# Kernel tuning notes

Measured on AMD Instinct MI355X. Metric: run time of the kernel, lower is better.

Reference implementation:

```python
import jax, jax.numpy as jnp
import numpy as np

B, N = 8, 2048          # clouds x points per cloud
M1, M2 = 1024, 256      # centroids after ratio 0.5, then 0.25
K = 64                  # max_num_neighbors
R1, R2 = 0.2, 0.4       # radii
CURV_K = 10             # knn for curvature
CURV_SCALAR = 10.0      # Net(curvature_scalar)
NEG = -1e30


def _sqdist(a, b):
    # squared pairwise distances [len(a), len(b)] without an [.,.,3] intermediate
    return jnp.sum(a * a, -1)[:, None] + jnp.sum(b * b, -1)[None, :] - 2.0 * (a @ b.T)


def _mlp3(x, Wa, ba, Wb, bb, Wc, bc):
    # torch_geometric MLP: Linear+ReLU hidden layers, plain last layer
    h = jax.nn.relu(x @ Wa + ba)
    h = jax.nn.relu(h @ Wb + bb)
    return h @ Wc + bc


def _curvature(pos):
    # per-point surface variation lambda_min / sum(lambda) over k-NN covariance
    d2 = _sqdist(pos, pos)                        # [N,N]
    _, idx = jax.lax.top_k(-d2, CURV_K)           # k nearest (incl. self)
    nbr = pos[idx]                                # [N,k,3]
    c = nbr - jnp.mean(nbr, 1, keepdims=True)
    cov = jnp.einsum('nki,nkj->nij', c, c) / CURV_K
    ev = jnp.linalg.eigvalsh(cov)                 # ascending
    return ev[:, 0] / (jnp.sum(ev, -1) + 1e-8)


def _fps_weighted(pos, curv, m):
    # farthest point sampling, min-distance score weighted by curvature
    w = 1.0 + CURV_SCALAR * curv
    d0 = jnp.sum((pos - pos[0]) ** 2, -1)
    def step(min_d2, _):
        i = jnp.argmax(min_d2 * w)
        nd = jnp.sum((pos - pos[i]) ** 2, -1)
        return jnp.minimum(min_d2, nd), i
    _, rest = jax.lax.scan(step, d0, None, length=m - 1)
    return jnp.concatenate([jnp.zeros((1,), rest.dtype), rest])


def _sa(x, pos, curv, m, r, params):
    # SAModule: weighted FPS -> radius grouping (cap K) -> PointNetConv (gather, MLP, max)
    idx = _fps_weighted(pos, curv, m)
    cpos = pos[idx]                               # [m,3]
    d2 = _sqdist(cpos, pos)                       # [m,N]
    score = jnp.where(d2 <= r * r, -d2, NEG)
    vals, nidx = jax.lax.top_k(score, K)          # up to K nearest within radius
    mask = vals > NEG * 0.5                       # [m,K]
    rel = pos[nidx] - cpos[:, None, :]            # [m,K,3]
    feats = rel if x is None else jnp.concatenate([x[nidx], rel], -1)
    msg = _mlp3(feats, *params)                   # [m,K,F]
    msg = jnp.where(mask[:, :, None], msg, NEG)
    out = jnp.max(msg, 1)                         # scatter-max aggregation
    out = jnp.where(jnp.any(mask, 1)[:, None], out, 0.0)  # empty groups -> 0
    return out, cpos, curv[idx]


def _forward(pos, W1a, b1a, W1b, b1b, W1c, b1c, W2a, b2a, W2b, b2b, W2c, b2c,
             W3a, b3a, W3b, b3b, W3c, b3c, Wh1, bh1, Wh2, bh2, Wh3, bh3):
    p1 = (W1a, b1a, W1b, b1b, W1c, b1c)
    p2 = (W2a, b2a, W2b, b2b, W2c, b2c)
    p3 = (W3a, b3a, W3b, b3b, W3c, b3c)
    def cloud(p):
        curv = _curvature(p)
        x1, pos1, c1 = _sa(None, p, curv, M1, R1, p1)
        x2, pos2, _ = _sa(x1, pos1, c1, M2, R2, p2)
        g = _mlp3(jnp.concatenate([x2, pos2], -1), *p3)   # [M2,1024]
        return jnp.max(g, 0)                              # global max pool
    gfeat = jax.vmap(cloud)(pos.reshape(B, N, 3))          # [B,1024]
    logits = _mlp3(gfeat, Wh1, bh1, Wh2, bh2, Wh3, bh3)    # dropout (eval) = id
    return jax.nn.log_softmax(logits, -1)


_LAYERS = [("W1a", "b1a", 3, 64), ("W1b", "b1b", 64, 64), ("W1c", "b1c", 64, 128),
           ("W2a", "b2a", 131, 128), ("W2b", "b2b", 128, 128), ("W2c", "b2c", 128, 256),
           ("W3a", "b3a", 259, 256), ("W3b", "b3b", 256, 512), ("W3c", "b3c", 512, 1024),
           ("Wh1", "bh1", 1024, 512), ("Wh2", "bh2", 512, 256), ("Wh3", "bh3", 256, 10)]


def setup_inputs() -> dict:
    key = jax.random.key(0)
    ks = iter(jax.random.split(key, 2 * len(_LAYERS) + 1))
    inp = {"pos": jax.random.uniform(next(ks), (B * N, 3), jnp.float32)}
    for wn, bn, fi, fo in _LAYERS:
        inp[wn] = jax.random.normal(next(ks), (fi, fo), jnp.float32) / np.sqrt(fi)
        inp[bn] = jnp.zeros((fo,), jnp.float32)
    return inp


def reference(pos, W1a, b1a, W1b, b1b, W1c, b1c, W2a, b2a, W2b, b2b, W2c, b2c,
              W3a, b3a, W3b, b3b, W3c, b3c, Wh1, bh1, Wh2, bh2, Wh3, bh3):
    return _forward(pos, W1a, b1a, W1b, b1b, W1c, b1c, W2a, b2a, W2b, b2b, W2c, b2c,
                    W3a, b3a, W3b, b3b, W3c, b3c, Wh1, bh1, Wh2, bh2, Wh3, bh3)
```

## Files before the change

kernel.cpp:

```cpp
#include <hip/hip_runtime.h>
#include <hip/hip_fp16.h>
#include <math.h>

#define TID threadIdx.x

typedef _Float16 h2vec __attribute__((ext_vector_type(2)));
typedef _Float16 f16x8 __attribute__((ext_vector_type(8)));
typedef float f32x4 __attribute__((ext_vector_type(4)));
typedef float f32x2v __attribute__((ext_vector_type(2)));

#if __has_builtin(__builtin_elementwise_fma)
#define EFMA(a, b, c) __builtin_elementwise_fma((a), (b), (c))
#else
static __device__ __forceinline__ f32x2v EFMA(f32x2v a, f32x2v b, f32x2v c) {
    f32x2v r;
    r.x = fmaf(a.x, b.x, c.x);
    r.y = fmaf(a.y, b.y, c.y);
    return r;
}
#endif

static __device__ __forceinline__ float fdot2(unsigned a, unsigned b, float c) {
    h2vec av, bv;
    __builtin_memcpy(&av, &a, 4);
    __builtin_memcpy(&bv, &b, 4);
    return __builtin_amdgcn_fdot2(av, bv, c, false);
}

static __device__ __forceinline__ unsigned packh2(float a, float b) {
    __half2 hh = __floats2half2_rn(a, b);
    unsigned u;
    __builtin_memcpy(&u, &hh, 4);
    return u;
}

static __device__ __forceinline__ unsigned encf(float f) {
    unsigned u = __float_as_uint(f);
    return (u >> 31) ? ~u : (u | 0x80000000u);
}
static __device__ __forceinline__ float decf(unsigned e) {
    unsigned u = (e >> 31) ? (e & 0x7fffffffu) : ~e;
    return __uint_as_float(u);
}

static __device__ __forceinline__ int wave_sum(int v) {
    v += __builtin_amdgcn_update_dpp(0, v, 0x111, 0xf, 0xf, true);
    v += __builtin_amdgcn_update_dpp(0, v, 0x112, 0xf, 0xf, true);
    v += __builtin_amdgcn_update_dpp(0, v, 0x114, 0xf, 0xf, true);
    v += __builtin_amdgcn_update_dpp(0, v, 0x118, 0xf, 0xf, true);
    v += __builtin_amdgcn_update_dpp(0, v, 0x142, 0xf, 0xf, true);
    v += __builtin_amdgcn_update_dpp(0, v, 0x143, 0xf, 0xf, true);
    return __builtin_amdgcn_readlane(v, 63);
}

template <int CTRL>
static __device__ __forceinline__ unsigned long long dpp_max_u64(unsigned long long k) {
    int lo = (int)(unsigned)(k & 0xffffffffULL);
    int hi = (int)(unsigned)(k >> 32);
    int lo2 = __builtin_amdgcn_update_dpp(0, lo, CTRL, 0xf, 0xf, true);
    int hi2 = __builtin_amdgcn_update_dpp(0, hi, CTRL, 0xf, 0xf, true);
    unsigned long long k2 = ((unsigned long long)(unsigned)hi2 << 32) | (unsigned)lo2;
    return k2 > k ? k2 : k;
}

static __device__ __forceinline__ void pack_slot(const float* __restrict__ W,
                                                 unsigned* __restrict__ out,
                                                 int K, int ncols, int t) {
    int lane = t & 63;
    int frag = t >> 6;
    int nct = ncols >> 4;
    int ks = frag / nct, ct = frag - ks * nct;
    int kbase = (ks << 5) + ((lane >> 4) << 3);
    int cc = (ct << 4) + (lane & 15);
    unsigned o[4];
#pragma unroll
    for (int i = 0; i < 4; ++i) {
        int k0 = kbase + 2 * i, k1 = kbase + 2 * i + 1;
        float f0 = (k0 < K) ? W[(size_t)k0 * ncols + cc] : 0.f;
        float f1 = (k1 < K) ? W[(size_t)k1 * ncols + cc] : 0.f;
        o[i] = packh2(f0, f1);
    }
    *(uint4*)&out[(size_t)t * 4] = make_uint4(o[0], o[1], o[2], o[3]);
}

__global__ __launch_bounds__(256) void curv_kernel(const float* __restrict__ pos,
                                                   float* __restrict__ curv) {
    __shared__ float4 sp[2048];
    __shared__ float smd[64][40];
    __shared__ int smi[64][40];
    int cloud = blockIdx.x >> 5;
    int base = cloud << 11;
    for (int j = TID; j < 2048; j += 256) {
        const float* p = pos + (size_t)(base + j) * 3;
        float x = p[0], y = p[1], z = p[2];
        sp[j] = make_float4(x, y, z, fmaf(x, x, fmaf(y, y, z * z)));
    }
    __syncthreads();
    int pt = TID >> 2;
    int sub = TID & 3;
    int li = ((blockIdx.x & 31) << 6) + pt;
    float4 pi = sp[li];
    float bd[10];
    int bi[10];
#pragma unroll
    for (int t = 0; t < 10; ++t) { bd[t] = 3.0e38f; bi[t] = 0; }
    int j0 = sub << 9;
    for (int jj = 0; jj < 512; ++jj) {
        int j = j0 + jj;
        float4 pj = sp[j];
        float dot = fmaf(pi.x, pj.x, fmaf(pi.y, pj.y, pi.z * pj.z));
        float d2 = pi.w + pj.w - 2.0f * dot;
        if (d2 < bd[9]) {
            bd[9] = d2; bi[9] = j;
#pragma unroll
            for (int t = 9; t > 0; --t) {
                if (bd[t] < bd[t - 1]) {
                    float td = bd[t]; bd[t] = bd[t - 1]; bd[t - 1] = td;
                    int ti = bi[t]; bi[t] = bi[t - 1]; bi[t - 1] = ti;
                }
            }
        }
    }
#pragma unroll
    for (int t = 0; t < 10; ++t) {
        smd[pt][sub * 10 + t] = bd[t];
        smi[pt][sub * 10 + t] = bi[t];
    }
    __syncthreads();
    float d0 = smd[pt][0], d1 = smd[pt][10], d2h = smd[pt][20], d3 = smd[pt][30];
    int i0 = smi[pt][0], i1 = smi[pt][10], i2 = smi[pt][20], i3 = smi[pt][30];
    int h0 = 0, h1 = 0, h2c = 0, h3 = 0;
    int mbi[10];
#pragma unroll
    for (int t = 0; t < 10; ++t) {
        bool a01 = (d1 < d0) || (d1 == d0 && i1 < i0);
        float dA = a01 ? d1 : d0; int iA = a01 ? i1 : i0;
        bool a23 = (d3 < d2h) || (d3 == d2h && i3 < i2);
        float dB = a23 ? d3 : d2h; int iB = a23 ? i3 : i2;
        bool ab = (dB < dA) || (dB == dA && iB < iA);
        mbi[t] = ab ? iB : iA;
        if (ab) {
            if (a23) { ++h3; d3 = (h3 < 10) ? smd[pt][30 + h3] : 3.0e38f;
                       i3 = (h3 < 10) ? smi[pt][30 + h3] : 0x7fffffff; }
            else     { ++h2c; d2h = (h2c < 10) ? smd[pt][20 + h2c] : 3.0e38f;
                       i2 = (h2c < 10) ? smi[pt][20 + h2c] : 0x7fffffff; }
        } else {
            if (a01) { ++h1; d1 = (h1 < 10) ? smd[pt][10 + h1] : 3.0e38f;
                       i1 = (h1 < 10) ? smi[pt][10 + h1] : 0x7fffffff; }
            else     { ++h0; d0 = (h0 < 10) ? smd[pt][h0] : 3.0e38f;
                       i0 = (h0 < 10) ? smi[pt][h0] : 0x7fffffff; }
        }
    }
    if (sub != 0) return;
    double sx = 0, sy = 0, sz = 0;
#pragma unroll
    for (int t = 0; t < 10; ++t) { float4 p = sp[mbi[t]]; sx += p.x; sy += p.y; sz += p.z; }
    double mx = sx / 10.0, my = sy / 10.0, mz = sz / 10.0;
    double cxx = 0, cxy = 0, cxz = 0, cyy = 0, cyz = 0, czz = 0;
#pragma unroll
    for (int t = 0; t < 10; ++t) {
        float4 p = sp[mbi[t]];
        double dx = p.x - mx, dy = p.y - my, dz = p.z - mz;
        cxx += dx * dx; cxy += dx * dy; cxz += dx * dz;
        cyy += dy * dy; cyz += dy * dz; czz += dz * dz;
    }
    cxx /= 10.0; cxy /= 10.0; cxz /= 10.0; cyy /= 10.0; cyz /= 10.0; czz /= 10.0;
    double q = (cxx + cyy + czz) / 3.0;
    double b00 = cxx - q, b11 = cyy - q, b22 = czz - q;
    double p2 = b00 * b00 + b11 * b11 + b22 * b22 +
                2.0 * (cxy * cxy + cxz * cxz + cyz * cyz);
    double lmin;
    if (p2 <= 0.0) {
        lmin = q;
    } else {
        double p = sqrt(p2 / 6.0);
        double inv = 1.0 / p;
        double c00 = b00 * inv, c01 = cxy * inv, c02 = cxz * inv;
        double c11 = b11 * inv, c12 = cyz * inv, c22 = b22 * inv;
        double detB = c00 * (c11 * c22 - c12 * c12)
                    - c01 * (c01 * c22 - c12 * c02)
                    + c02 * (c01 * c12 - c11 * c02);
        double r = 0.5 * detB;
        r = fmin(1.0, fmax(-1.0, r));
        double phi = acos(r) / 3.0;
        lmin = q + 2.0 * p * cos(phi + 2.0943951023931953);
    }
    double s3 = cxx + cyy + czz;
    curv[base + li] = (float)(lmin / (s3 + 1e-8));
}

template <int N, int M, int SLOTS>
static __device__ void fps_body(
    const float* __restrict__ srcpos, int stride, const float* __restrict__ srccurv,
    int cloud, float4* __restrict__ outPos, float* __restrict__ outCurv,
    float* __restrict__ outA, int ldA,
    float4* sp, int* sidx, unsigned long long* rec ) {
    constexpr int PAIRS = SLOTS / 2;
    const float* cp = srcpos + (size_t)cloud * N * stride;
    for (int j = TID; j < N; j += 256)
        sp[j] = make_float4(cp[j * stride], cp[j * stride + 1], cp[j * stride + 2], 0.f);
    if (TID == 0) sidx[0] = 0;
    __syncthreads();
    f32x2v px[PAIRS], py[PAIRS], pz[PAIRS], md[PAIRS], wvv[PAIRS];
#pragma unroll
    for (int s = 0; s < PAIRS; ++s) {
        int p0 = ((2 * s) << 8) + TID, p1 = ((2 * s + 1) << 8) + TID;
        float4 q0 = sp[p0], q1 = sp[p1];
        px[s].x = q0.x; px[s].y = q1.x;
        py[s].x = q0.y; py[s].y = q1.y;
        pz[s].x = q0.z; pz[s].y = q1.z;
        md[s].x = 3.0e38f; md[s].y = 3.0e38f;
        wvv[s].x = fmaf(10.0f, srccurv[cloud * N + p0], 1.0f);
        wvv[s].y = fmaf(10.0f, srccurv[cloud * N + p1], 1.0f);
    }
    int lane = TID & 63, w4 = TID >> 6;
    float4 c0 = sp[0];
    float cx = c0.x, cy = c0.y, cz = c0.z;
    for (int t = 1; t < M; ++t) {
        f32x2v cxv, cyv, czv;
        cxv.x = cx; cxv.y = cx; cyv.x = cy; cyv.y = cy; czv.x = cz; czv.y = cz;
        unsigned long long kk[PAIRS];
#pragma unroll
        for (int s = 0; s < PAIRS; ++s) {
            f32x2v dx = px[s] - cxv, dy = py[s] - cyv, dz = pz[s] - czv;
            f32x2v nd = EFMA(dx, dx, EFMA(dy, dy, dz * dz));
            f32x2v m2 = __builtin_elementwise_min(md[s], nd);
            md[s] = m2;
            f32x2v sc = m2 * wvv[s];
            unsigned long long k0 =
                ((unsigned long long)__float_as_uint(sc.x) << 32) |
                (unsigned)(2047 - (((2 * s) << 8) + TID));
            unsigned long long k1 =
                ((unsigned long long)__float_as_uint(sc.y) << 32) |
                (unsigned)(2047 - (((2 * s + 1) << 8) + TID));
            kk[s] = k0 > k1 ? k0 : k1;
        }
        unsigned long long k = kk[0];
#pragma unroll
        for (int s = 1; s < PAIRS; ++s) k = kk[s] > k ? kk[s] : k;
        k = dpp_max_u64<0x111>(k);
        k = dpp_max_u64<0x112>(k);
        k = dpp_max_u64<0x114>(k);
        k = dpp_max_u64<0x118>(k);
        k = dpp_max_u64<0x142>(k);
        k = dpp_max_u64<0x143>(k);
        int pbase = (t & 1) << 2;
        if (lane == 63) rec[pbase | w4] = k;
        __syncthreads();
        unsigned long long k0 = rec[pbase + 0];
        unsigned long long k1 = rec[pbase + 1];
        unsigned long long k2 = rec[pbase + 2];
        unsigned long long k3 = rec[pbase + 3];
        unsigned long long ka = k0 > k1 ? k0 : k1;
        unsigned long long kb = k2 > k3 ? k2 : k3;
        unsigned long long km = ka > kb ? ka : kb;
        int nbix = 2047 - (int)(unsigned)(km & 0xffffffffULL);
        if (TID == 0) sidx[t] = nbix;
        float4 cc = sp[nbix];
        cx = cc.x; cy = cc.y; cz = cc.z;
    }
    __syncthreads();
    for (int j = TID; j < M; j += 256) {
        int id = sidx[j];
        float4 qv = sp[id];
        outPos[cloud * M + j] = qv;
        if (outCurv) outCurv[cloud * M + j] = srccurv[cloud * N + id];
        if (outA) {
            float* a = outA + (size_t)(cloud * M + j) * ldA;
            a[256] = qv.x; a[257] = qv.y; a[258] = qv.z;
        }
    }
}

__global__ __launch_bounds__(256, 1) void fps1_pack_kernel(
    const float* __restrict__ pos, const float* __restrict__ curv,
    float4* __restrict__ pos1, float* __restrict__ curv1,
    const float* __restrict__ Wc, const float* __restrict__ Wa,
    const float* __restrict__ Wb, const float* __restrict__ W3a,
    const float* __restrict__ W3b, const float* __restrict__ W3c,
    const float* __restrict__ W1b, const float* __restrict__ W1c,
    unsigned* __restrict__ WcH, unsigned* __restrict__ WaH,
    unsigned* __restrict__ WbH, unsigned* __restrict__ W3aH,
    unsigned* __restrict__ W3bH, unsigned* __restrict__ W3cH,
    unsigned* __restrict__ W1bH, unsigned* __restrict__ W1cH,
    unsigned* __restrict__ gfeatE) {
    __shared__ float4 sp[2048];
    __shared__ int sidx[1024];
    __shared__ unsigned long long rec[8];
    if (blockIdx.x < 8) {
        fps_body<2048, 1024, 8>(pos, 3, curv, blockIdx.x, pos1, curv1, nullptr, 0,
                                sp, sidx, rec);
        return;
    }
    int b = blockIdx.x - 8;
    if (b == 0)
        for (int i = TID; i < 8192; i += 256) gfeatE[i] = 0u;
    if (b < 16)        pack_slot(Wc,  WcH,  128, 256,  b * 256 + TID);
    else if (b < 26)   pack_slot(Wa,  WaH,  131, 128,  (b - 16) * 256 + TID);
    else if (b < 34)   pack_slot(Wb,  WbH,  128, 128,  (b - 26) * 256 + TID);
    else if (b < 70)   pack_slot(W3a, W3aH, 259, 256,  (b - 34) * 256 + TID);
    else if (b < 134)  pack_slot(W3b, W3bH, 256, 512,  (b - 70) * 256 + TID);
    else if (b < 390)  pack_slot(W3c, W3cH, 512, 1024, (b - 134) * 256 + TID);
    else if (b < 392)  pack_slot(W1b, W1bH, 64, 64,    (b - 390) * 256 + TID);
    else               pack_slot(W1c, W1cH, 64, 128,   (b - 392) * 256 + TID);
}

template <int NCH>
static __device__ __forceinline__ int select_k64_reg(
    const unsigned* __restrict__ ck, const int* __restrict__ ci,
    int c, int lane, int* sel, int* nbOut) {
    if (c <= 64) {
        *nbOut = c;
        return (lane < c) ? ci[lane] : 0;
    }
    unsigned long long kq[NCH];
    bool act[NCH];
#pragma unroll
    for (int q = 0; q < NCH; ++q) {
        int idx = (q << 6) + lane;
        bool v = idx < c;
        act[q] = v;
        kq[q] = v ? (((unsigned long long)ck[idx] << 32) | (unsigned)ci[idx]) : 0ULL;
    }
    int excess = c - 64;
    if (excess <= 24) {
        for (int r = 0; r < excess; ++r) {
            unsigned long long k = 0;
#pragma unroll
            for (int q = 0; q < NCH; ++q) {
                unsigned long long kc = act[q] ? kq[q] : 0ULL;
                k = kc > k ? kc : k;
            }
            k = dpp_max_u64<0x111>(k);
            k = dpp_max_u64<0x112>(k);
            k = dpp_max_u64<0x114>(k);
            k = dpp_max_u64<0x118>(k);
            k = dpp_max_u64<0x142>(k);
            k = dpp_max_u64<0x143>(k);
            unsigned klo = (unsigned)__builtin_amdgcn_readlane(
                (int)(unsigned)(k & 0xffffffffULL), 63);
            unsigned khi = (unsigned)__builtin_amdgcn_readlane(
                (int)(unsigned)(k >> 32), 63);
            unsigned long long km = ((unsigned long long)khi << 32) | klo;
#pragma unroll
            for (int q = 0; q < NCH; ++q)
                if (act[q] && kq[q] == km) act[q] = false;
        }
    } else {
        unsigned T = 0;
        for (int bit = 31; bit >= 0; --bit) {
            unsigned mid = T | (1u << bit);
            int cl = 0;
#pragma unroll
            for (int q = 0; q < NCH; ++q)
                cl += (act[q] && (unsigned)(kq[q] >> 32) < mid) ? 1 : 0;
            if (wave_sum(cl) < 64) T = mid;
        }
        int cl = 0;
#pragma unroll
        for (int q = 0; q < NCH; ++q)
            cl += (act[q] && (unsigned)(kq[q] >> 32) < T) ? 1 : 0;
        int need = 64 - wave_sum(cl);
        int TI = 0;
        for (int bit = 11; bit >= 0; --bit) {
            int mid = TI | (1 << bit);
            int ce = 0;
#pragma unroll
            for (int q = 0; q < NCH; ++q)
                ce += (act[q] && (unsigned)(kq[q] >> 32) == T &&
                       (int)(unsigned)(kq[q] & 0xffffffffULL) < mid) ? 1 : 0;
            if (wave_sum(ce) < need) TI = mid;
        }
#pragma unroll
        for (int q = 0; q < NCH; ++q) {
            unsigned hi = (unsigned)(kq[q] >> 32);
            int lo = (int)(unsigned)(kq[q] & 0xffffffffULL);
            act[q] = act[q] && (hi < T || (hi == T && lo <= TI));
        }
    }
    int base = 0;
#pragma unroll
    for (int q = 0; q < NCH; ++q) {
        unsigned long long m = __ballot(act[q]);
        if (act[q]) {
            int off = __popcll(m & ((1ULL << lane) - 1));
            sel[base + off] = (int)(unsigned)(kq[q] & 0xffffffffULL);
        }
        base += __popcll(m);
    }
    *nbOut = 64;
    return sel[lane];
}

union U1 {
    struct {
        float4 sp[2048];
        unsigned ck[4][256];
        int ci[4][256];
        int sel[4][64];
    } p;
    unsigned hs[4][2304];
};

static __device__ void conv1_body(
    int bid, U1& u,
    const float* __restrict__ pos, const float4* __restrict__ pos1,
    const float* __restrict__ W1, const float* __restrict__ B1,
    const unsigned* __restrict__ W1bH, const float* __restrict__ B2,
    const unsigned* __restrict__ W1cH, const float* __restrict__ B3,
    float* __restrict__ x1) {
    __shared__ int nbs[4];
    int cloud = bid >> 8;
    int w4 = TID >> 6, lane = TID & 63;
    int quad = lane >> 4, l15 = lane & 15;
    int centb = (bid & 255) << 2;
    int g = (cloud << 10) + centb + w4;
    int base = cloud << 11;
    for (int j = TID; j < 2048; j += 256) {
        const float* p = pos + (size_t)(base + j) * 3;
        u.p.sp[j] = make_float4(p[0], p[1], p[2], 0.f);
    }
    __syncthreads();
    float4 cq = pos1[g];
    double cx = cq.x, cy = cq.y, cz = cq.z;
    int cnt = 0;
    for (int s = 0; s < 32; ++s) {
        int j = (s << 6) + lane;
        float4 pj = u.p.sp[j];
        double dx = (double)pj.x - cx, dy = (double)pj.y - cy, dz = (double)pj.z - cz;
        double d2 = dx * dx + dy * dy + dz * dz;
        bool in = (d2 <= 0.2 * 0.2);
        unsigned long long m = __ballot(in);
        if (in) {
            int p = cnt + __popcll(m & ((1ULL << lane) - 1));
            if (p < 256) {
                u.p.ck[w4][p] = __float_as_uint((float)d2);
                u.p.ci[w4][p] = j;
            }
        }
        cnt += __popcll(m);
    }
    int c = min(cnt, 256);
    int nb;
    int idxn = select_k64_reg<4>(u.p.ck[w4], u.p.ci[w4], c, lane, u.p.sel[w4], &nb);
    if (lane == 0) nbs[w4] = nb;
    float4 pn = u.p.sp[idxn];
    float rx = pn.x - cq.x, ry = pn.y - cq.y, rz = pn.z - cq.z;
    float h1[64];
#pragma unroll
    for (int cc2 = 0; cc2 < 64; ++cc2) {
        float v = fmaf(rx, W1[cc2], fmaf(ry, W1[64 + cc2], fmaf(rz, W1[128 + cc2], B1[cc2])));
        h1[cc2] = fmaxf(v, 0.f);
    }
    __syncthreads();
    {
        unsigned* row = &u.hs[w4][lane * 36];
#pragma unroll
        for (int q = 0; q < 8; ++q) {
            *(uint4*)&row[q << 2] =
                make_uint4(packh2(h1[8 * q + 0], h1[8 * q + 1]),
                           packh2(h1[8 * q + 2], h1[8 * q + 3]),
                           packh2(h1[8 * q + 4], h1[8 * q + 5]),
                           packh2(h1[8 * q + 6], h1[8 * q + 7]));
        }
    }
    __syncthreads();
    {
        f16x8 bfrag[2][4];
#pragma unroll
        for (int ks = 0; ks < 2; ++ks)
#pragma unroll
            for (int ct = 0; ct < 4; ++ct) {
                uint4 bv = *(const uint4*)&W1bH[(size_t)(
                    (((ks << 2) | ct) << 6) | lane) << 2];
                __builtin_memcpy(&bfrag[ks][ct], &bv, 16);
            }
        f16x8 af[4][2];
#pragma unroll
        for (int rt = 0; rt < 4; ++rt)
#pragma unroll
            for (int ks = 0; ks < 2; ++ks) {
                uint4 av = *(const uint4*)&u.hs[w4][((rt << 4) + l15) * 36 +
                                                    (((ks << 2) | quad) << 2)];
                __builtin_memcpy(&af[rt][ks], &av, 16);
            }
        float ba4[4];
#pragma unroll
        for (int ct = 0; ct < 4; ++ct) ba4[ct] = B2[(ct << 4) + l15];
#pragma unroll
        for (int rt = 0; rt < 4; ++rt) {
#pragma unroll
            for (int ct = 0; ct < 4; ++ct) {
                f32x4 acc = {0.f, 0.f, 0.f, 0.f};
#pragma unroll
                for (int ks = 0; ks < 2; ++ks)
                    acc = __builtin_amdgcn_mfma_f32_16x16x32_f16(
                        af[rt][ks], bfrag[ks][ct], acc, 0, 0, 0);
#pragma unroll
                for (int r = 0; r < 4; ++r) {
                    float v = fmaxf(acc[r] + ba4[ct], 0.f);
                    float vp = __shfl_xor(v, 1, 64);
                    if (!(l15 & 1)) {
                        int rowi = (rt << 4) + (quad << 2) + r;
                        u.hs[w4][rowi * 36 + (ct << 3) + (l15 >> 1)] = packh2(v, vp);
                    }
                }
            }
        }
    }
    __syncthreads();
    {
        int ct2 = w4 << 1;
        f16x8 cfrag[2][2];
#pragma unroll
        for (int ctl = 0; ctl < 2; ++ctl)
#pragma unroll
            for (int ks = 0; ks < 2; ++ks) {
                uint4 bv = *(const uint4*)&W1cH[(size_t)(
                    (((ks << 3) | (ct2 + ctl)) << 6) | lane) << 2];
                __builtin_memcpy(&cfrag[ctl][ks], &bv, 16);
            }
#pragma unroll 1
        for (int cent = 0; cent < 4; ++cent) {
            int nbc = nbs[cent];
            float runM[2][4];
#pragma unroll
            for (int ctl = 0; ctl < 2; ++ctl)
#pragma unroll
                for (int r = 0; r < 4; ++r) runM[ctl][r] = -1e30f;
#pragma unroll
            for (int rt = 0; rt < 4; ++rt) {
                f16x8 af[2];
#pragma unroll
                for (int ks = 0; ks < 2; ++ks) {
                    uint4 av = *(const uint4*)&u.hs[cent][((rt << 4) + l15) * 36 +
                                                          (((ks << 2) | quad) << 2)];
                    __builtin_memcpy(&af[ks], &av, 16);
                }
#pragma unroll
                for (int ctl = 0; ctl < 2; ++ctl) {
                    f32x4 acc = {0.f, 0.f, 0.f, 0.f};
#pragma unroll
                    for (int ks = 0; ks < 2; ++ks)
                        acc = __builtin_amdgcn_mfma_f32_16x16x32_f16(
                            af[ks], cfrag[ctl][ks], acc, 0, 0, 0);
                    int nb0 = (rt << 4) + (quad << 2);
#pragma unroll
                    for (int r = 0; r < 4; ++r) {
                        float v = (nb0 + r < nbc) ? acc[r] : -1e30f;
                        runM[ctl][r] = fmaxf(runM[ctl][r], v);
                    }
                }
            }
#pragma unroll
            for (int ctl = 0; ctl < 2; ++ctl) {
                float m = fmaxf(fmaxf(runM[ctl][0], runM[ctl][1]),
                                fmaxf(runM[ctl][2], runM[ctl][3]));
                m = fmaxf(m, __shfl_xor(m, 16, 64));
                m = fmaxf(m, __shfl_xor(m, 32, 64));
                if (lane < 16) {
                    int cc = ((ct2 + ctl) << 4) | l15;
                    x1[(size_t)((cloud << 10) + centb + cent) * 128 + cc] = m + B3[cc];
                }
            }
        }
    }
}

union UM {
    U1 c;
    struct {
        float4 sp[1024];
        unsigned long long rec[8];
        int sidx[256];
    } f;
};

__global__ __launch_bounds__(256, 3) void fps2_conv1_kernel(
    const float* __restrict__ pos, const float4* __restrict__ pos1,
    const float* __restrict__ curv1, float4* __restrict__ pos2,
    float* __restrict__ Abuf,
    const float* __restrict__ W1, const float* __restrict__ B1,
    const unsigned* __restrict__ W1bH, const float* __restrict__ B2,
    const unsigned* __restrict__ W1cH, const float* __restrict__ B3,
    float* __restrict__ x1) {
    __shared__ UM u;
    if (blockIdx.x < 8) {
        fps_body<1024, 256, 4>((const float*)pos1, 4, curv1, blockIdx.x, pos2,
                               nullptr, Abuf, 260, u.f.sp, u.f.sidx, u.f.rec);
    } else {
        conv1_body(blockIdx.x - 8, u.c, pos, pos1, W1, B1, W1bH, B2, W1cH, B3, x1);
    }
}

union U2 {
    struct {
        float4 sp[1024];
        unsigned ck[4][512];
        int ci[4][512];
        int sel[4][64];
    } p;
    unsigned xs[4][5376];
};

__global__ __launch_bounds__(256, 1) void conv2_kernel(
    const float4* __restrict__ pos1, const float4* __restrict__ pos2,
    const float* __restrict__ x1,
    const unsigned* __restrict__ WaH, const float* __restrict__ Ba,
    const unsigned* __restrict__ WbH, const float* __restrict__ Bb,
    const unsigned* __restrict__ WcH, const float* __restrict__ Bc,
    float* __restrict__ Aout) {
    __shared__ U2 u;
    __shared__ unsigned h1s[4][4352];
    __shared__ int nbs[4];
    int cloud = blockIdx.x >> 6;
    int w4 = TID >> 6, lane = TID & 63;
    int centb = (blockIdx.x & 63) << 2;
    int g = (cloud << 8) + centb + w4;
    int quad = lane >> 4, l15 = lane & 15;
    for (int j = TID; j < 1024; j += 256) u.p.sp[j] = pos1[(cloud << 10) + j];
    __syncthreads();
    float4 cq = pos2[g];
    double cx = cq.x, cy = cq.y, cz = cq.z;
    int cnt = 0;
    for (int s = 0; s < 16; ++s) {
        int j = (s << 6) + lane;
        float4 pj = u.p.sp[j];
        double dx = (double)pj.x - cx, dy = (double)pj.y - cy, dz = (double)pj.z - cz;
        double d2 = dx * dx + dy * dy + dz * dz;
        bool in = (d2 <= 0.4 * 0.4);
        unsigned long long m = __ballot(in);
        if (in) {
            int p = cnt + __popcll(m & ((1ULL << lane) - 1));
            if (p < 512) {
                u.p.ck[w4][p] = __float_as_uint((float)d2);
                u.p.ci[w4][p] = j;
            }
        }
        cnt += __popcll(m);
    }
    int c = min(cnt, 512);
    int nb;
    int idxn = select_k64_reg<8>(u.p.ck[w4], u.p.ci[w4], c, lane, u.p.sel[w4], &nb);
    if (lane == 0) nbs[w4] = nb;
    float4 pn = u.p.sp[idxn];
    float rx = pn.x - cq.x, ry = pn.y - cq.y, rz = pn.z - cq.z;
    __syncthreads();
    {
        const float4* xr = (const float4*)(x1 + (size_t)((cloud << 10) + idxn) * 128);
        unsigned* row = &u.xs[w4][lane * 84];
#pragma unroll
        for (int q = 0; q < 16; ++q) {
            float4 a = xr[q * 2], b = xr[q * 2 + 1];
            *(uint4*)&row[q << 2] = make_uint4(packh2(a.x, a.y), packh2(a.z, a.w),
                                               packh2(b.x, b.y), packh2(b.z, b.w));
        }
        *(uint4*)&row[64] = make_uint4(packh2(rx, ry), packh2(rz, 0.f), 0u, 0u);
        *(uint4*)&row[68] = make_uint4(0u, 0u, 0u, 0u);
        *(uint4*)&row[72] = make_uint4(0u, 0u, 0u, 0u);
        *(uint4*)&row[76] = make_uint4(0u, 0u, 0u, 0u);
    }
    float ba8[8];
#pragma unroll
    for (int ct = 0; ct < 8; ++ct) ba8[ct] = Ba[(ct << 4) + l15];
#pragma unroll 1
    for (int ct = 0; ct < 8; ++ct) {
        f16x8 bfrag[5];
#pragma unroll
        for (int ks = 0; ks < 5; ++ks) {
            uint4 bv = *(const uint4*)&WaH[(size_t)((((ks << 3) | ct) << 6) | lane) << 2];
            __builtin_memcpy(&bfrag[ks], &bv, 16);
        }
#pragma unroll
        for (int rt = 0; rt < 4; ++rt) {
            f32x4 acc = {0.f, 0.f, 0.f, 0.f};
#pragma unroll
            for (int ks = 0; ks < 5; ++ks) {
                f16x8 af;
                uint4 av = *(const uint4*)&u.xs[w4][((rt << 4) + l15) * 84 +
                                                    (((ks << 2) + quad) << 2)];
                __builtin_memcpy(&af, &av, 16);
                acc = __builtin_amdgcn_mfma_f32_16x16x32_f16(af, bfrag[ks], acc, 0, 0, 0);
            }
#pragma unroll
            for (int r = 0; r < 4; ++r) {
                float v = fmaxf(acc[r] + ba8[ct], 0.f);
                float vp = __shfl_xor(v, 1, 64);
                if (!(l15 & 1)) {
                    int rowi = (rt << 4) + (quad << 2) + r;
                    h1s[w4][rowi * 68 + (ct << 3) + (l15 >> 1)] = packh2(v, vp);
                }
            }
        }
    }
    unsigned* h2w = &u.xs[w4][0];
#pragma unroll
    for (int ct = 0; ct < 8; ++ct) ba8[ct] = Bb[(ct << 4) + l15];
#pragma unroll 1
    for (int ct = 0; ct < 8; ++ct) {
        f16x8 bfrag[4];
#pragma unroll
        for (int ks = 0; ks < 4; ++ks) {
            uint4 bv = *(const uint4*)&WbH[(size_t)((((ks << 3) | ct) << 6) | lane) << 2];
            __builtin_memcpy(&bfrag[ks], &bv, 16);
        }
#pragma unroll
        for (int rt = 0; rt < 4; ++rt) {
            f32x4 acc = {0.f, 0.f, 0.f, 0.f};
#pragma unroll
            for (int ks = 0; ks < 4; ++ks) {
                f16x8 af;
                uint4 av = *(const uint4*)&h1s[w4][((rt << 4) + l15) * 68 +
                                                   (((ks << 2) + quad) << 2)];
                __builtin_memcpy(&af, &av, 16);
                acc = __builtin_amdgcn_mfma_f32_16x16x32_f16(af, bfrag[ks], acc, 0, 0, 0);
            }
#pragma unroll
            for (int r = 0; r < 4; ++r) {
                float v = fmaxf(acc[r] + ba8[ct], 0.f);
                float vp = __shfl_xor(v, 1, 64);
                if (!(l15 & 1)) {
                    int rowi = (rt << 4) + (quad << 2) + r;
                    int d = (ct << 3) + (l15 >> 1);
                    int ch = d >> 2, din = d & 3;
                    h2w[(rowi << 6) + ((ch ^ (rowi & 15)) << 2) + din] = packh2(v, vp);
                }
            }
        }
    }
    __syncthreads();
    int ctb = w4 << 2;
    f16x8 cfrag[4][4];
#pragma unroll
    for (int ct = 0; ct < 4; ++ct)
#pragma unroll
        for (int ks = 0; ks < 4; ++ks) {
            uint4 bv = *(const uint4*)&WcH[(size_t)((((ks << 4) | (ctb + ct)) << 6) | lane) << 2];
            __builtin_memcpy(&cfrag[ct][ks], &bv, 16);
        }
#pragma unroll 1
    for (int cent = 0; cent < 4; ++cent) {
        const unsigned* h2r = &u.xs[cent][0];
        int nbc = nbs[cent];
        float runM[4][4];
#pragma unroll
        for (int ct = 0; ct < 4; ++ct)
#pragma unroll
            for (int r = 0; r < 4; ++r) runM[ct][r] = -1e30f;
#pragma unroll
        for (int rt = 0; rt < 4; ++rt) {
            int nl = (rt << 4) + l15;
            f16x8 afrag[4];
#pragma unroll
            for (int ks = 0; ks < 4; ++ks) {
                int cp = ((ks << 2) | quad) ^ l15;
                uint4 av = *(const uint4*)&h2r[(nl << 6) + (cp << 2)];
                __builtin_memcpy(&afrag[ks], &av, 16);
            }
#pragma unroll
            for (int ct = 0; ct < 4; ++ct) {
                f32x4 acc = {0.f, 0.f, 0.f, 0.f};
#pragma unroll
                for (int ks = 0; ks < 4; ++ks)
                    acc = __builtin_amdgcn_mfma_f32_16x16x32_f16(afrag[ks], cfrag[ct][ks],
                                                                 acc, 0, 0, 0);
                int nb0 = (rt << 4) + (quad << 2);
#pragma unroll
                for (int r = 0; r < 4; ++r) {
                    float v = (nb0 + r < nbc) ? acc[r] : -1e30f;
                    runM[ct][r] = fmaxf(runM[ct][r], v);
                }
            }
        }
#pragma unroll
        for (int ct = 0; ct < 4; ++ct) {
            float m = fmaxf(fmaxf(runM[ct][0], runM[ct][1]),
                            fmaxf(runM[ct][2], runM[ct][3]));
            m = fmaxf(m, __shfl_xor(m, 16, 64));
            m = fmaxf(m, __shfl_xor(m, 32, 64));
            if (lane < 16) {
                int cc = ((ctb + ct) << 4) | l15;
                Aout[(size_t)((cloud << 8) + centb + cent) * 260 + cc] = m + Bc[cc];
            }
        }
    }
}

__global__ __launch_bounds__(256) void gemm_mfma2(
    const float* __restrict__ A, int lda, const unsigned* __restrict__ Bp, int nct,
    const float* __restrict__ bias, float* __restrict__ C, int ldc, int K,
    int relu, unsigned* __restrict__ gmax) {
    int w = (blockIdx.x << 2) + (TID >> 6);
    int ncg = nct >> 3;
    int rs = w / ncg, cg = w - rs * ncg;
    int r0 = rs << 4, ct0 = cg << 3;
    int lane = TID & 63, quad = lane >> 4, l15 = lane & 15;
    f32x4 acc[8];
#pragma unroll
    for (int ct = 0; ct < 8; ++ct) acc[ct] = (f32x4){0.f, 0.f, 0.f, 0.f};
    const float* ar = A + (size_t)(r0 + l15) * lda;
    int nks = (K + 31) >> 5;
    for (int ks = 0; ks < nks; ++ks) {
        int kb = (ks << 5) + (quad << 3);
        f16x8 af;
        if (kb + 8 <= K) {
            float4 a0 = *(const float4*)(ar + kb);
            float4 a1 = *(const float4*)(ar + kb + 4);
            uint4 av = make_uint4(packh2(a0.x, a0.y), packh2(a0.z, a0.w),
                                  packh2(a1.x, a1.y), packh2(a1.z, a1.w));
            __builtin_memcpy(&af, &av, 16);
        } else {
            float f[8];
#pragma unroll
            for (int j = 0; j < 8; ++j) f[j] = (kb + j < K) ? ar[kb + j] : 0.f;
            uint4 av = make_uint4(packh2(f[0], f[1]), packh2(f[2], f[3]),
                                  packh2(f[4], f[5]), packh2(f[6], f[7]));
            __builtin_memcpy(&af, &av, 16);
        }
#pragma unroll
        for (int ct = 0; ct < 8; ++ct) {
            uint4 bv = *(const uint4*)&Bp[(size_t)(((ks * nct + ct0 + ct) << 6) | lane) << 2];
            f16x8 bf;
            __builtin_memcpy(&bf, &bv, 16);
            acc[ct] = __builtin_amdgcn_mfma_f32_16x16x32_f16(af, bf, acc[ct], 0, 0, 0);
        }
    }
    if (!gmax) {
#pragma unroll
        for (int ct = 0; ct < 8; ++ct) {
            int col = ((ct0 + ct) << 4) + l15;
            float bb = bias[col];
#pragma unroll
            for (int r = 0; r < 4; ++r) {
                int row = r0 + (quad << 2) + r;
                float v = acc[ct][r] + bb;
                if (relu) v = fmaxf(v, 0.f);
                C[(size_t)row * ldc + col] = v;
            }
        }
    } else {
        int cloud = r0 >> 8;
#pragma unroll
        for (int ct = 0; ct < 8; ++ct) {
            int col = ((ct0 + ct) << 4) + l15;
            float bb = bias[col];
            float m = fmaxf(fmaxf(acc[ct][0], acc[ct][1]),
                            fmaxf(acc[ct][2], acc[ct][3])) + bb;
            m = fmaxf(m, __shfl_xor(m, 16, 64));
            m = fmaxf(m, __shfl_xor(m, 32, 64));
            if (quad == 0) atomicMax(&gmax[(cloud << 10) + col], encf(m));
        }
    }
}

__global__ __launch_bounds__(128) void head1_kernel(
    const unsigned* __restrict__ gfeatE,
    const float* __restrict__ Wh1, const float* __restrict__ bh1,
    float* __restrict__ s1g) {
    int cloud = TID >> 4;
    int col = (blockIdx.x << 4) + (TID & 15);
    float v = bh1[col];
    const unsigned* ge = gfeatE + (cloud << 10);
    for (int i = 0; i < 1024; ++i)
        v = fmaf(decf(ge[i]), Wh1[i * 512 + col], v);
    s1g[(cloud << 9) + col] = fmaxf(v, 0.f);
}

__global__ __launch_bounds__(128) void head2_kernel(
    const float* __restrict__ s1g,
    const float* __restrict__ Wh2, const float* __restrict__ bh2,
    float* __restrict__ s2g) {
    int cloud = TID >> 4;
    int col = (blockIdx.x << 4) + (TID & 15);
    float v = bh2[col];
    const float* s1 = s1g + (cloud << 9);
    for (int i = 0; i < 512; ++i)
        v = fmaf(s1[i], Wh2[i * 256 + col], v);
    s2g[(cloud << 8) + col] = fmaxf(v, 0.f);
}

__global__ __launch_bounds__(64) void head3_kernel(
    const float* __restrict__ s2g,
    const float* __restrict__ Wh3, const float* __restrict__ bh3,
    float* __restrict__ out) {
    __shared__ float lg[10];
    int cloud = blockIdx.x;
    const float* s2 = s2g + (cloud << 8);
    if (TID < 10) {
        float v = bh3[TID];
        for (int i = 0; i < 256; ++i) v = fmaf(s2[i], Wh3[i * 10 + TID], v);
        lg[TID] = v;
    }
    __syncthreads();
    if (TID == 0) {
        float mx = lg[0];
        for (int i = 1; i < 10; ++i) mx = fmaxf(mx, lg[i]);
        float s = 0.f;
        for (int i = 0; i < 10; ++i) s += expf(lg[i] - mx);
        float lse = mx + logf(s);
        for (int i = 0; i < 10; ++i) out[cloud * 10 + i] = lg[i] - lse;
    }
}

extern "C" void kernel_launch(void* const* d_in, const int* in_sizes, int n_in,
                              void* d_out, int out_size, void* d_ws, size_t ws_size,
                              hipStream_t stream) {
    (void)in_sizes; (void)n_in; (void)out_size; (void)ws_size;
    const float* pos = (const float*)d_in[0];
    const float* W1a = (const float*)d_in[1];  const float* b1a = (const float*)d_in[2];
    const float* W1b = (const float*)d_in[3];  const float* b1b = (const float*)d_in[4];
    const float* W1c = (const float*)d_in[5];  const float* b1c = (const float*)d_in[6];
    const float* W2a = (const float*)d_in[7];  const float* b2a = (const float*)d_in[8];
    const float* W2b = (const float*)d_in[9];  const float* b2b = (const float*)d_in[10];
    const float* W2c = (const float*)d_in[11]; const float* b2c = (const float*)d_in[12];
    const float* W3a = (const float*)d_in[13]; const float* b3a = (const float*)d_in[14];
    const float* W3b = (const float*)d_in[15]; const float* b3b = (const float*)d_in[16];
    const float* W3c = (const float*)d_in[17]; const float* b3c = (const float*)d_in[18];
    const float* Wh1 = (const float*)d_in[19]; const float* bh1 = (const float*)d_in[20];
    const float* Wh2 = (const float*)d_in[21]; const float* bh2 = (const float*)d_in[22];
    const float* Wh3 = (const float*)d_in[23]; const float* bh3 = (const float*)d_in[24];

    char* ws = (char*)d_ws;
    float*    curv   = (float*)(ws + 0);
    float4*   pos1   = (float4*)(ws + 98304);
    float*    curv1  = (float*)(ws + 229376);
    float4*   pos2   = (float4*)(ws + 270336);
    unsigned* gfeatE = (unsigned*)(ws + 303104);
    unsigned* WcH    = (unsigned*)(ws + 335872);
    unsigned* WaH    = (unsigned*)(ws + 401408);
    unsigned* WbH    = (unsigned*)(ws + 442368);
    unsigned* W1bH   = (unsigned*)(ws + 475136);
    unsigned* W1cH   = (unsigned*)(ws + 483328);
    float*    x1     = (float*)(ws + 524288);
    float*    Abuf   = (float*)(ws + 4718592);
    float*    h1g    = (float*)(ws + 6848512);
    unsigned* W3aH   = (unsigned*)(ws + 8945664);
    unsigned* W3bH   = (unsigned*)(ws + 9093120);
    unsigned* W3cH   = (unsigned*)(ws + 9355264);
    float*    h2g    = x1;
    float*    s1g    = h1g;
    float*    s2g    = h1g + 4096;

    curv_kernel<<<256, 256, 0, stream>>>(pos, curv);
    fps1_pack_kernel<<<404, 256, 0, stream>>>(pos, curv, pos1, curv1,
                                              W2c, W2a, W2b, W3a, W3b, W3c,
                                              W1b, W1c,
                                              WcH, WaH, WbH, W3aH, W3bH, W3cH,
                                              W1bH, W1cH,
                                              gfeatE);
    fps2_conv1_kernel<<<2056, 256, 0, stream>>>(pos, pos1, curv1, pos2, Abuf,
                                                W1a, b1a, W1bH, b1b, W1cH, b1c, x1);
    conv2_kernel<<<512, 256, 0, stream>>>(pos1, pos2, x1, WaH, b2a, WbH, b2b, WcH, b2c,
                                          Abuf);
    gemm_mfma2<<<64, 256, 0, stream>>>(Abuf, 260, W3aH, 16, b3a, h1g, 256,
                                       259, 1, nullptr);
    gemm_mfma2<<<128, 256, 0, stream>>>(h1g, 256, W3bH, 32, b3b, h2g, 512,
                                        256, 1, nullptr);
    gemm_mfma2<<<256, 256, 0, stream>>>(h2g, 512, W3cH, 64, b3c, nullptr, 0,
                                        512, 0, gfeatE);
    head1_kernel<<<32, 128, 0, stream>>>(gfeatE, Wh1, bh1, s1g);
    head2_kernel<<<16, 128, 0, stream>>>(s1g, Wh2, bh2, s2g);
    head3_kernel<<<8, 64, 0, stream>>>(s2g, Wh3, bh3, (float*)d_out);
}
```

Baseline: 1.068 ms.

## Split conv2 work across two waves per centroid with 512-thread blocks

Doubles the conv2 block to 8 waves so each centroid gets two waves. One wave of each pair does the radius search and top-64 selection, and the pair then splits the feature gather, the first two MLP layers' column tiles, and the final layer's output columns. Two extra block barriers are added, and the selection wave's latency is now exposed while its partner waits. Per-wave registers drop, but LDS use stays the same and only one block fits per CU.

```diff
diff --git a/kernel.cpp b/kernel.cpp
--- a/kernel.cpp
+++ b/kernel.cpp
@@ -598,12 +598,11 @@
         float4 sp[1024];
         unsigned ck[4][512];
         int ci[4][512];
-        int sel[4][64];
     } p;
     unsigned xs[4][5376];
 };
 
-__global__ __launch_bounds__(256, 1) void conv2_kernel(
+__global__ __launch_bounds__(512, 1) void conv2_kernel(
     const float4* __restrict__ pos1, const float4* __restrict__ pos2,
     const float* __restrict__ x1,
     const unsigned* __restrict__ WaH, const float* __restrict__ Ba,
@@ -612,59 +611,75 @@
     float* __restrict__ Aout) {
     __shared__ U2 u;
     __shared__ unsigned h1s[4][4352];
+    __shared__ int selS[4][64];
     __shared__ int nbs[4];
     int cloud = blockIdx.x >> 6;
-    int w4 = TID >> 6, lane = TID & 63;
+    int w8 = TID >> 6, lane = TID & 63;
     int centb = (blockIdx.x & 63) << 2;
-    int g = (cloud << 8) + centb + w4;
+    int cent = w8 >> 1;
+    bool wA = (w8 & 1) == 0;
+    int g = (cloud << 8) + centb + cent;
     int quad = lane >> 4, l15 = lane & 15;
-    for (int j = TID; j < 1024; j += 256) u.p.sp[j] = pos1[(cloud << 10) + j];
+    for (int j = TID; j < 1024; j += 512) u.p.sp[j] = pos1[(cloud << 10) + j];
     __syncthreads();
     float4 cq = pos2[g];
-    double cx = cq.x, cy = cq.y, cz = cq.z;
-    int cnt = 0;
-    for (int s = 0; s < 16; ++s) {
-        int j = (s << 6) + lane;
-        float4 pj = u.p.sp[j];
-        double dx = (double)pj.x - cx, dy = (double)pj.y - cy, dz = (double)pj.z - cz;
-        double d2 = dx * dx + dy * dy + dz * dz;
-        bool in = (d2 <= 0.4 * 0.4);
-        unsigned long long m = __ballot(in);
-        if (in) {
-            int p = cnt + __popcll(m & ((1ULL << lane) - 1));
-            if (p < 512) {
-                u.p.ck[w4][p] = __float_as_uint((float)d2);
-                u.p.ci[w4][p] = j;
-            }
-        }
-        cnt += __popcll(m);
-    }
-    int c = min(cnt, 512);
-    int nb;
-    int idxn = select_k64_reg<8>(u.p.ck[w4], u.p.ci[w4], c, lane, u.p.sel[w4], &nb);
-    if (lane == 0) nbs[w4] = nb;
-    float4 pn = u.p.sp[idxn];
-    float rx = pn.x - cq.x, ry = pn.y - cq.y, rz = pn.z - cq.z;
-    __syncthreads();
+    int idxn = 0;
+    float rx = 0.f, ry = 0.f, rz = 0.f;
+    if (wA) {
+        double cx = cq.x, cy = cq.y, cz = cq.z;
+        int cnt = 0;
+        for (int s = 0; s < 16; ++s) {
+            int j = (s << 6) + lane;
+            float4 pj = u.p.sp[j];
+            double dx = (double)pj.x - cx, dy = (double)pj.y - cy, dz = (double)pj.z - cz;
+            double d2 = dx * dx + dy * dy + dz * dz;
+            bool in = (d2 <= 0.4 * 0.4);
+            unsigned long long m = __ballot(in);
+            if (in) {
+                int p = cnt + __popcll(m & ((1ULL << lane) - 1));
+                if (p < 512) {
+                    u.p.ck[cent][p] = __float_as_uint((float)d2);
+                    u.p.ci[cent][p] = j;
+                }
+            }
+            cnt += __popcll(m);
+        }
+        int c = min(cnt, 512);
+        int nb;
+        idxn = select_k64_reg<8>(u.p.ck[cent], u.p.ci[cent], c, lane, selS[cent], &nb);
+        if (lane == 0) nbs[cent] = nb;
+        selS[cent][lane] = idxn;
+        float4 pn = u.p.sp[idxn];
+        rx = pn.x - cq.x; ry = pn.y - cq.y; rz = pn.z - cq.z;
+    }
+    __syncthreads();
+    if (!wA) idxn = selS[cent][lane];
     {
         const float4* xr = (const float4*)(x1 + (size_t)((cloud << 10) + idxn) * 128);
-        unsigned* row = &u.xs[w4][lane * 84];
-#pragma unroll
-        for (int q = 0; q < 16; ++q) {
+        unsigned* row = &u.xs[cent][lane * 84];
+        int q0 = wA ? 0 : 8;
+#pragma unroll
+        for (int qi = 0; qi < 8; ++qi) {
+            int q = q0 + qi;
             float4 a = xr[q * 2], b = xr[q * 2 + 1];
             *(uint4*)&row[q << 2] = make_uint4(packh2(a.x, a.y), packh2(a.z, a.w),
                                                packh2(b.x, b.y), packh2(b.z, b.w));
         }
-        *(uint4*)&row[64] = make_uint4(packh2(rx, ry), packh2(rz, 0.f), 0u, 0u);
-        *(uint4*)&row[68] = make_uint4(0u, 0u, 0u, 0u);
-        *(uint4*)&row[72] = make_uint4(0u, 0u, 0u, 0u);
-        *(uint4*)&row[76] = make_uint4(0u, 0u, 0u, 0u);
-    }
-    float ba8[8];
-#pragma unroll
-    for (int ct = 0; ct < 8; ++ct) ba8[ct] = Ba[(ct << 4) + l15];
+        if (wA) {
+            *(uint4*)&row[64] = make_uint4(packh2(rx, ry), packh2(rz, 0.f), 0u, 0u);
+            *(uint4*)&row[68] = make_uint4(0u, 0u, 0u, 0u);
+            *(uint4*)&row[72] = make_uint4(0u, 0u, 0u, 0u);
+            *(uint4*)&row[76] = make_uint4(0u, 0u, 0u, 0u);
+        }
+    }
+    __syncthreads();
+    int ctb4 = (w8 & 1) << 2;
+    float ba4[4];
+#pragma unroll
+    for (int c4 = 0; c4 < 4; ++c4) ba4[c4] = Ba[((ctb4 + c4) << 4) + l15];
 #pragma unroll 1
-    for (int ct = 0; ct < 8; ++ct) {
+    for (int c4 = 0; c4 < 4; ++c4) {
+        int ct = ctb4 + c4;
         f16x8 bfrag[5];
 #pragma unroll
         for (int ks = 0; ks < 5; ++ks) {
@@ -677,27 +692,29 @@
 #pragma unroll
             for (int ks = 0; ks < 5; ++ks) {
                 f16x8 af;
-                uint4 av = *(const uint4*)&u.xs[w4][((rt << 4) + l15) * 84 +
-                                                    (((ks << 2) + quad) << 2)];
+                uint4 av = *(const uint4*)&u.xs[cent][((rt << 4) + l15) * 84 +
+                                                      (((ks << 2) + quad) << 2)];
                 __builtin_memcpy(&af, &av, 16);
                 acc = __builtin_amdgcn_mfma_f32_16x16x32_f16(af, bfrag[ks], acc, 0, 0, 0);
             }
 #pragma unroll
             for (int r = 0; r < 4; ++r) {
-                float v = fmaxf(acc[r] + ba8[ct], 0.f);
+                float v = fmaxf(acc[r] + ba4[c4], 0.f);
                 float vp = __shfl_xor(v, 1, 64);
                 if (!(l15 & 1)) {
                     int rowi = (rt << 4) + (quad << 2) + r;
-                    h1s[w4][rowi * 68 + (ct << 3) + (l15 >> 1)] = packh2(v, vp);
+                    h1s[cent][rowi * 68 + (ct << 3) + (l15 >> 1)] = packh2(v, vp);
                 }
             }
         }
     }
-    unsigned* h2w = &u.xs[w4][0];
-#pragma unroll
-    for (int ct = 0; ct < 8; ++ct) ba8[ct] = Bb[(ct << 4) + l15];
+    __syncthreads();
+    unsigned* h2w = &u.xs[cent][0];
+#pragma unroll
+    for (int c4 = 0; c4 < 4; ++c4) ba4[c4] = Bb[((ctb4 + c4) << 4) + l15];
 #pragma unroll 1
-    for (int ct = 0; ct < 8; ++ct) {
+    for (int c4 = 0; c4 < 4; ++c4) {
+        int ct = ctb4 + c4;
         f16x8 bfrag[4];
 #pragma unroll
         for (int ks = 0; ks < 4; ++ks) {
@@ -710,14 +727,14 @@
 #pragma unroll
             for (int ks = 0; ks < 4; ++ks) {
                 f16x8 af;
-                uint4 av = *(const uint4*)&h1s[w4][((rt << 4) + l15) * 68 +
-                                                   (((ks << 2) + quad) << 2)];
+                uint4 av = *(const uint4*)&h1s[cent][((rt << 4) + l15) * 68 +
+                                                     (((ks << 2) + quad) << 2)];
                 __builtin_memcpy(&af, &av, 16);
                 acc = __builtin_amdgcn_mfma_f32_16x16x32_f16(af, bfrag[ks], acc, 0, 0, 0);
             }
 #pragma unroll
             for (int r = 0; r < 4; ++r) {
-                float v = fmaxf(acc[r] + ba8[ct], 0.f);
+                float v = fmaxf(acc[r] + ba4[c4], 0.f);
                 float vp = __shfl_xor(v, 1, 64);
                 if (!(l15 & 1)) {
                     int rowi = (rt << 4) + (quad << 2) + r;
@@ -729,24 +746,24 @@
         }
     }
     __syncthreads();
-    int ctb = w4 << 2;
-    f16x8 cfrag[4][4];
-#pragma unroll
-    for (int ct = 0; ct < 4; ++ct)
+    int ctb2 = w8 << 1;
+    f16x8 cfrag[2][4];
+#pragma unroll
+    for (int ctl = 0; ctl < 2; ++ctl)
 #pragma unroll
         for (int ks = 0; ks < 4; ++ks) {
-            uint4 bv = *(const uint4*)&WcH[(size_t)((((ks << 4) | (ctb + ct)) << 6) | lane) << 2];
-            __builtin_memcpy(&cfrag[ct][ks], &bv, 16);
+            uint4 bv = *(const uint4*)&WcH[(size_t)((((ks << 4) | (ctb2 + ctl)) << 6) | lane) << 2];
+            __builtin_memcpy(&cfrag[ctl][ks], &bv, 16);
         }
 #pragma unroll 1
-    for (int cent = 0; cent < 4; ++cent) {
-        const unsigned* h2r = &u.xs[cent][0];
-        int nbc = nbs[cent];
-        float runM[4][4];
-#pragma unroll
-        for (int ct = 0; ct < 4; ++ct)
-#pragma unroll
-            for (int r = 0; r < 4; ++r) runM[ct][r] = -1e30f;
+    for (int ce = 0; ce < 4; ++ce) {
+        const unsigned* h2r = &u.xs[ce][0];
+        int nbc = nbs[ce];
+        float runM[2][4];
+#pragma unroll
+        for (int ctl = 0; ctl < 2; ++ctl)
+#pragma unroll
+            for (int r = 0; r < 4; ++r) runM[ctl][r] = -1e30f;
 #pragma unroll
         for (int rt = 0; rt < 4; ++rt) {
             int nl = (rt << 4) + l15;
@@ -758,29 +775,29 @@
                 __builtin_memcpy(&afrag[ks], &av, 16);
             }
 #pragma unroll
-            for (int ct = 0; ct < 4; ++ct) {
+            for (int ctl = 0; ctl < 2; ++ctl) {
                 f32x4 acc = {0.f, 0.f, 0.f, 0.f};
 #pragma unroll
                 for (int ks = 0; ks < 4; ++ks)
-                    acc = __builtin_amdgcn_mfma_f32_16x16x32_f16(afrag[ks], cfrag[ct][ks],
+                    acc = __builtin_amdgcn_mfma_f32_16x16x32_f16(afrag[ks], cfrag[ctl][ks],
                                                                  acc, 0, 0, 0);
                 int nb0 = (rt << 4) + (quad << 2);
 #pragma unroll
                 for (int r = 0; r < 4; ++r) {
                     float v = (nb0 + r < nbc) ? acc[r] : -1e30f;
-                    runM[ct][r] = fmaxf(runM[ct][r], v);
+                    runM[ctl][r] = fmaxf(runM[ctl][r], v);
                 }
             }
         }
 #pragma unroll
-        for (int ct = 0; ct < 4; ++ct) {
-            float m = fmaxf(fmaxf(runM[ct][0], runM[ct][1]),
-                            fmaxf(runM[ct][2], runM[ct][3]));
+        for (int ctl = 0; ctl < 2; ++ctl) {
+            float m = fmaxf(fmaxf(runM[ctl][0], runM[ctl][1]),
+                            fmaxf(runM[ctl][2], runM[ctl][3]));
             m = fmaxf(m, __shfl_xor(m, 16, 64));
             m = fmaxf(m, __shfl_xor(m, 32, 64));
             if (lane < 16) {
-                int cc = ((ctb + ct) << 4) | l15;
-                Aout[(size_t)((cloud << 8) + centb + cent) * 260 + cc] = m + Bc[cc];
+                int cc = ((ctb2 + ctl) << 4) | l15;
+                Aout[(size_t)((cloud << 8) + centb + ce) * 260 + cc] = m + Bc[cc];
             }
         }
     }
@@ -950,7 +967,7 @@
                                               gfeatE);
     fps2_conv1_kernel<<<2056, 256, 0, stream>>>(pos, pos1, curv1, pos2, Abuf,
                                                 W1a, b1a, W1bH, b1b, W1cH, b1c, x1);
-    conv2_kernel<<<512, 256, 0, stream>>>(pos1, pos2, x1, WaH, b2a, WbH, b2b, WcH, b2c,
+    conv2_kernel<<<512, 512, 0, stream>>>(pos1, pos2, x1, WaH, b2a, WbH, b2b, WcH, b2c,
                                           Abuf);
     gemm_mfma2<<<64, 256, 0, stream>>>(Abuf, 260, W3aH, 16, b3a, h1g, 256,
                                        259, 1, nullptr);
```

Result: no change. 1.048 ms, median of 2 (-1.9%).
